# Kernel optimization log

Hardware: AMD Instinct MI355X
Metric: run time of the kernel (lower is better)

The kernel has to match this reference:

```python
import jax, jax.numpy as jnp
import numpy as np

T, B = 128, 256
E, H, C = 128, 1024, 10
VOCAB = 10


def setup_inputs() -> dict:
    key = jax.random.key(0)
    ks = jax.random.split(key, 12)
    x = jax.random.randint(ks[0], (T, B), 0, VOCAB)
    emb = jax.random.normal(ks[1], (VOCAB, E), dtype=jnp.float32)
    Wgx = jax.random.normal(ks[2], (E, H), dtype=jnp.float32) / np.sqrt(E)
    Wgh = jax.random.normal(ks[3], (H, H), dtype=jnp.float32) / np.sqrt(H)
    Wix = jax.random.normal(ks[4], (E, H), dtype=jnp.float32) / np.sqrt(E)
    Wih = jax.random.normal(ks[5], (H, H), dtype=jnp.float32) / np.sqrt(H)
    Wfx = jax.random.normal(ks[6], (E, H), dtype=jnp.float32) / np.sqrt(E)
    Wfh = jax.random.normal(ks[7], (H, H), dtype=jnp.float32) / np.sqrt(H)
    Wox = jax.random.normal(ks[8], (E, H), dtype=jnp.float32) / np.sqrt(E)
    Woh = jax.random.normal(ks[9], (H, H), dtype=jnp.float32) / np.sqrt(H)
    Wph = jax.random.normal(ks[10], (H, C), dtype=jnp.float32) / np.sqrt(H)
    bg = jnp.zeros((H,), jnp.float32)
    bi = jnp.zeros((H,), jnp.float32)
    bf = jnp.zeros((H,), jnp.float32)
    bo = jnp.zeros((H,), jnp.float32)
    bp = jnp.zeros((C,), jnp.float32)
    return dict(x=x, emb=emb, Wgx=Wgx, Wgh=Wgh, Wix=Wix, Wih=Wih, Wfx=Wfx,
                Wfh=Wfh, Wox=Wox, Woh=Woh, bg=bg, bi=bi, bf=bf, bo=bo,
                Wph=Wph, bp=bp)


def reference(x, emb, Wgx, Wgh, Wix, Wih, Wfx, Wfh, Wox, Woh,
              bg, bi, bf, bo, Wph, bp):
    Bsz = x.shape[1]
    Hn = Wgh.shape[0]
    # Fuse the 8 gate matmuls into 2 GEMMs per step (same math, concat order g,i,f,o)
    Wx = jnp.concatenate([Wgx, Wix, Wfx, Wox], axis=1)  # [E, 4H]
    Wh = jnp.concatenate([Wgh, Wih, Wfh, Woh], axis=1)  # [H, 4H]
    b = jnp.concatenate([bg, bi, bf, bo], axis=0)        # [4H]

    def step(carry, xt):
        state, hidden = carry
        e = emb[xt]                                      # [B, E]
        pre = e @ Wx + hidden @ Wh + b                   # [B, 4H]
        g = jnp.tanh(pre[:, :Hn])
        i = jax.nn.sigmoid(pre[:, Hn:2 * Hn])
        f = jax.nn.sigmoid(pre[:, 2 * Hn:3 * Hn])
        o = jax.nn.sigmoid(pre[:, 3 * Hn:])
        state = g * i + state * f
        hidden = jnp.tanh(state) * o
        return (state, hidden), None

    init = (jnp.zeros((Bsz, Hn), jnp.float32), jnp.zeros((Bsz, Hn), jnp.float32))
    (state, hidden), _ = jax.lax.scan(step, init, x)
    # Original detaches hidden/state before the output projection
    hidden = jax.lax.stop_gradient(hidden)
    return hidden @ Wph + bp                             # [B, C]
```

## Files before the change

kernel.cpp:

```cpp
#include <hip/hip_runtime.h>

typedef __bf16 bf16;
typedef __bf16 bf16x8 __attribute__((ext_vector_type(8)));
typedef float  f32x4  __attribute__((ext_vector_type(4)));
typedef int    i32x4  __attribute__((ext_vector_type(4)));

#define T_STEPS 128
#define BATCH   256
#define HD      1024
#define N4H     4096
#define EMB_D   128

#define MFMA_BF16(acc, Aop, Bop) \
    asm("v_mfma_f32_16x16x32_bf16 %0, %1, %2, %0" : "+v"(acc) : "a"(Aop), "v"(Bop))

__device__ __forceinline__ float fast_sigmoid(float x) {
    return 1.0f / (1.0f + __expf(-x));
}
__device__ __forceinline__ float fast_tanh(float x) {
    return 1.0f - 2.0f / (__expf(2.0f * x) + 1.0f);
}

__global__ void build_P(const float* __restrict__ emb,
                        const float* __restrict__ Wgx, const float* __restrict__ Wix,
                        const float* __restrict__ Wfx, const float* __restrict__ Wox,
                        const float* __restrict__ bg,  const float* __restrict__ bi,
                        const float* __restrict__ bfv, const float* __restrict__ bo,
                        float* __restrict__ P)
{
    int n = blockIdx.x * 256 + threadIdx.x;
    int v  = n >> 12;
    int nn = n & (N4H - 1);
    int hcol = nn >> 2, gate = nn & 3;
    const float* Wx = (gate == 0) ? Wgx : (gate == 1) ? Wix : (gate == 2) ? Wfx : Wox;
    const float* bb = (gate == 0) ? bg  : (gate == 1) ? bi  : (gate == 2) ? bfv : bo;
    float s = bb[hcol];
    for (int e = 0; e < EMB_D; ++e)
        s += emb[v * EMB_D + e] * Wx[e * HD + hcol];
    P[n] = s;
}

__global__ void build_W(const float* __restrict__ Wgh, const float* __restrict__ Wih,
                        const float* __restrict__ Wfh, const float* __restrict__ Woh,
                        bf16* __restrict__ WhpT)
{
    __shared__ float tile[64][65];
    int bid  = blockIdx.x;
    int gate = bid >> 8;
    int t2   = bid & 255;
    int kt = t2 >> 4, ht = t2 & 15;
    const float* W = (gate == 0) ? Wgh : (gate == 1) ? Wih : (gate == 2) ? Wfh : Woh;
    int tid = threadIdx.x;
    #pragma unroll
    for (int it = 0; it < 16; ++it) {
        int idx = it * 256 + tid;
        int kk = idx >> 6, hh = idx & 63;
        tile[kk][hh] = W[(size_t)(kt * 64 + kk) * HD + ht * 64 + hh];
    }
    __syncthreads();
    #pragma unroll
    for (int it = 0; it < 16; ++it) {
        int idx = it * 256 + tid;
        int hh = idx >> 6, kk = idx & 63;
        int n = (ht * 64 + hh) * 4 + gate;
        WhpT[(size_t)n * HD + kt * 64 + kk] = (bf16)tile[kk][hh];
    }
}

__global__ __launch_bounds__(512, 2)
void lstm_main(const int* __restrict__ x, const float* __restrict__ P,
               const bf16* __restrict__ WhpT, bf16* __restrict__ hbuf,
               int* __restrict__ ctl)
{
    __shared__ bf16  Blds[32][1024];
    __shared__ float red[8][64][9];
    __shared__ bf16  hst[32][34];
    __shared__ int   sj;

    const int tid  = threadIdx.x;
    const int lane = tid & 63;
    const int wid  = tid >> 6;
    const int w    = wid & 3;
    const int kh   = wid >> 2;
    const int frow = lane & 15;
    const int kgrp = lane >> 4;

    int xcc;
    asm("s_getreg_b32 %0, hwreg(HW_REG_XCC_ID)" : "=s"(xcc));
    const int g = xcc & 7;
    if (tid == 0)
        sj = __hip_atomic_fetch_add(ctl + 1024 + g * 16, 1,
                                    __ATOMIC_RELAXED, __HIP_MEMORY_SCOPE_AGENT) & 31;
    __syncthreads();
    const int j = sj;
    int* grpctr = ctl + g * 32;

    const int rowO = j * 128 + w * 32 + kh * 16 + frow;
    const int rowX = j * 128 + w * 32 + (1 - kh) * 16 + frow;
    const bf16* AbO = WhpT + (size_t)rowO * HD + kh * 512 + kgrp * 8;
    const bf16* AbX = WhpT + (size_t)rowX * HD + kh * 512 + kgrp * 8;
    i32x4 ArO[16], ArX[16];
    #pragma unroll
    for (int ks = 0; ks < 16; ++ks) {
        ArO[ks] = *(const i32x4*)(const void*)(AbO + ks * 32);
        ArX[ks] = *(const i32x4*)(const void*)(AbX + ks * 32);
    }
    #pragma unroll
    for (int ks = 0; ks < 16; ++ks)
        asm volatile("" : "+a"(ArO[ks]), "+a"(ArX[ks]));

    const int mr0 = g * 32 + frow;
    const int clc = w * 8 + kh * 4 + kgrp;
    const int pnb = j * 128 + clc * 4;
    const int xorf = frow & 7;
    char* BB = (char*)&Blds[0][0];
    float* rw = &red[0][0][0] + ((size_t)(wid ^ 4) * 64 + lane) * 9;
    const float* rr = &red[0][0][0] + ((size_t)wid * 64 + lane) * 9;
    const int* slot = grpctr + (lane & 31);

    float st0 = 0.f, st1 = 0.f;
    f32x4 accP0, accP1;
    {
        int xv0 = x[mr0], xv1 = x[mr0 + 16];
        accP0 = *(const f32x4*)(P + (size_t)xv0 * N4H + pnb);
        accP1 = *(const f32x4*)(P + (size_t)xv1 * N4H + pnb);
    }

    for (int t = 0; t < T_STEPS; ++t) {
        f32x4 accO0 = accP0, accO1 = accP1;
        f32x4 z = {0.f, 0.f, 0.f, 0.f};
        f32x4 accX0 = z, accX1 = z;

        if (t > 0) {
            if (wid == 0) {
                int cv; long guard = 0;
                do {
                    __builtin_amdgcn_s_sleep(1);
                    cv = __hip_atomic_load(slot, __ATOMIC_RELAXED,
                                           __HIP_MEMORY_SCOPE_AGENT);
                } while (!__all(cv >= t) && ++guard < (1L << 17));
            }
            __syncthreads();
            const char* src = (const char*)(hbuf + (size_t)(t & 1) * BATCH * HD
                                                 + (size_t)g * 32 * HD);
            f32x4 stg[8];
            #pragma unroll
            for (int i2 = 0; i2 < 8; ++i2)
                asm volatile("global_load_dwordx4 %0, %1, off sc0"
                             : "=v"(stg[i2]) : "v"(src + (i2 * 512 + tid) * 16));
            asm volatile("s_waitcnt vmcnt(0)" ::: "memory");
            #pragma unroll
            for (int i2 = 0; i2 < 8; ++i2) {
                int c = i2 * 512 + tid;
                int row = c >> 7, cg = c & 127;
                *(f32x4*)(BB + row * 2048 + ((cg ^ (row & 7)) << 4)) = stg[i2];
            }
            __syncthreads();
            #pragma unroll
            for (int ks = 0; ks < 16; ++ks) {
                int off = ((kh * 64 + ks * 4 + kgrp) ^ xorf) << 4;
                i32x4 b0 = *(const i32x4*)(BB + frow * 2048 + off);
                i32x4 b1 = *(const i32x4*)(BB + (frow + 16) * 2048 + off);
                MFMA_BF16(accO0, ArO[ks], b0);
                MFMA_BF16(accO1, ArO[ks], b1);
                MFMA_BF16(accX0, ArX[ks], b0);
                MFMA_BF16(accX1, ArX[ks], b1);
            }
        }

        rw[0] = accX0[0]; rw[1] = accX0[1]; rw[2] = accX0[2]; rw[3] = accX0[3];
        rw[4] = accX1[0]; rw[5] = accX1[1]; rw[6] = accX1[2]; rw[7] = accX1[3];
        __syncthreads();
        accO0[0] += rr[0]; accO0[1] += rr[1]; accO0[2] += rr[2]; accO0[3] += rr[3];
        accO1[0] += rr[4]; accO1[1] += rr[5]; accO1[2] += rr[6]; accO1[3] += rr[7];

        {
            float gg = fast_tanh(accO0[0]);
            float ii = fast_sigmoid(accO0[1]);
            float ff = fast_sigmoid(accO0[2]);
            float oo = fast_sigmoid(accO0[3]);
            float s = gg * ii + st0 * ff;
            st0 = s;
            hst[frow][clc] = (bf16)(fast_tanh(s) * oo);
        }
        {
            float gg = fast_tanh(accO1[0]);
            float ii = fast_sigmoid(accO1[1]);
            float ff = fast_sigmoid(accO1[2]);
            float oo = fast_sigmoid(accO1[3]);
            float s = gg * ii + st1 * ff;
            st1 = s;
            hst[frow + 16][clc] = (bf16)(fast_tanh(s) * oo);
        }

        if (t < T_STEPS - 1) {
            int xv0 = x[(t + 1) * BATCH + mr0], xv1 = x[(t + 1) * BATCH + mr0 + 16];
            accP0 = *(const f32x4*)(P + (size_t)xv0 * N4H + pnb);
            accP1 = *(const f32x4*)(P + (size_t)xv1 * N4H + pnb);
        }

        __syncthreads();
        {
            bf16* hout = hbuf + (size_t)((t + 1) & 1) * BATCH * HD;
            int r = tid >> 4, cp = (tid & 15) * 2;
            unsigned lo = (unsigned)__builtin_bit_cast(unsigned short, hst[r][cp]);
            unsigned hi = (unsigned)__builtin_bit_cast(unsigned short, hst[r][cp + 1]);
            unsigned pv = lo | (hi << 16);
            *(unsigned*)(hout + (size_t)(g * 32 + r) * HD + j * 32 + cp) = pv;
        }
        __syncthreads();
        if (tid == 0 && t < T_STEPS - 1)
            __hip_atomic_store(grpctr + j, t + 1,
                               __ATOMIC_RELAXED, __HIP_MEMORY_SCOPE_AGENT);
    }
}

__global__ void proj_out(const bf16* __restrict__ h, const float* __restrict__ Wph,
                         const float* __restrict__ bp, float* __restrict__ out)
{
    __shared__ float red[256][10];
    int b = blockIdx.x, tid = threadIdx.x;
    float acc[10];
    #pragma unroll
    for (int c = 0; c < 10; ++c) acc[c] = 0.f;
    for (int k = tid; k < HD; k += 256) {
        float hv = (float)h[(size_t)b * HD + k];
        #pragma unroll
        for (int c = 0; c < 10; ++c)
            acc[c] += hv * Wph[k * 10 + c];
    }
    #pragma unroll
    for (int c = 0; c < 10; ++c) red[tid][c] = acc[c];
    __syncthreads();
    for (int s = 128; s > 0; s >>= 1) {
        if (tid < s) {
            #pragma unroll
            for (int c = 0; c < 10; ++c) red[tid][c] += red[tid + s][c];
        }
        __syncthreads();
    }
    if (tid < 10) out[b * 10 + tid] = red[0][tid] + bp[tid];
}

extern "C" void kernel_launch(void* const* d_in, const int* in_sizes, int n_in,
                              void* d_out, int out_size, void* d_ws, size_t ws_size,
                              hipStream_t stream)
{
    const int*   x   = (const int*)  d_in[0];
    const float* emb = (const float*)d_in[1];
    const float* Wgx = (const float*)d_in[2];
    const float* Wgh = (const float*)d_in[3];
    const float* Wix = (const float*)d_in[4];
    const float* Wih = (const float*)d_in[5];
    const float* Wfx = (const float*)d_in[6];
    const float* Wfh = (const float*)d_in[7];
    const float* Wox = (const float*)d_in[8];
    const float* Woh = (const float*)d_in[9];
    const float* bg  = (const float*)d_in[10];
    const float* bi  = (const float*)d_in[11];
    const float* bfv = (const float*)d_in[12];
    const float* bo  = (const float*)d_in[13];
    const float* Wph = (const float*)d_in[14];
    const float* bp  = (const float*)d_in[15];

    char* ws = (char*)d_ws;
    bf16*  WhpT = (bf16*)ws;
    float* P    = (float*)(ws + 8388608);
    bf16*  hbuf = (bf16*)(ws + 8388608 + 163840);
    int*   ctl  = (int*)(ws + 8388608 + 163840 + 1048576);

    hipMemsetAsync(ctl, 0, 8192, stream);
    build_P<<<160, 256, 0, stream>>>(emb, Wgx, Wix, Wfx, Wox, bg, bi, bfv, bo, P);
    build_W<<<1024, 256, 0, stream>>>(Wgh, Wih, Wfh, Woh, WhpT);

    void* args[] = { (void*)&x, (void*)&P, (void*)&WhpT, (void*)&hbuf, (void*)&ctl };
    hipLaunchCooperativeKernel((void*)lstm_main, dim3(256), dim3(512), args, 0, stream);

    proj_out<<<256, 256, 0, stream>>>(hbuf, Wph, bp, (float*)d_out);
}
```

Baseline: 555.2 us.

## Split h staging by K-half and replace block barrier with per-half LDS flags

Each half of the workgroup (kh) now loads only the K-half of the hidden state that its own waves consume. Instead of a full __syncthreads after staging, the four waves in a half signal each other through per-wave LDS flags and spin on them. The s_sleep in the global poll loop is also removed to cut wake-up latency. The costs are busy-spinning waves competing for issue slots and reliance on LDS visibility ordering through volatile accesses and lgkmcnt waits.

```diff
diff --git a/kernel.cpp b/kernel.cpp
--- a/kernel.cpp
+++ b/kernel.cpp
@@ -75,6 +75,7 @@
     __shared__ bf16  Blds[32][1024];
     __shared__ float red[8][64][9];
     __shared__ bf16  hst[32][34];
+    __shared__ int   tflag[8];
     __shared__ int   sj;
 
     const int tid  = threadIdx.x;
@@ -84,6 +85,7 @@
     const int kh   = wid >> 2;
     const int frow = lane & 15;
     const int kgrp = lane >> 4;
+    const int ttid = tid & 255;
 
     int xcc;
     asm("s_getreg_b32 %0, hwreg(HW_REG_XCC_ID)" : "=s"(xcc));
@@ -91,6 +93,7 @@
     if (tid == 0)
         sj = __hip_atomic_fetch_add(ctl + 1024 + g * 16, 1,
                                     __ATOMIC_RELAXED, __HIP_MEMORY_SCOPE_AGENT) & 31;
+    if (tid < 8) tflag[tid] = 0;
     __syncthreads();
     const int j = sj;
     int* grpctr = ctl + g * 32;
@@ -135,7 +138,6 @@
             if (wid == 0) {
                 int cv; long guard = 0;
                 do {
-                    __builtin_amdgcn_s_sleep(1);
                     cv = __hip_atomic_load(slot, __ATOMIC_RELAXED,
                                            __HIP_MEMORY_SCOPE_AGENT);
                 } while (!__all(cv >= t) && ++guard < (1L << 17));
@@ -145,17 +147,32 @@
                                                  + (size_t)g * 32 * HD);
             f32x4 stg[8];
             #pragma unroll
-            for (int i2 = 0; i2 < 8; ++i2)
+            for (int it = 0; it < 8; ++it) {
+                int idx = it * 256 + ttid;
+                int row = idx >> 6, gg = idx & 63;
                 asm volatile("global_load_dwordx4 %0, %1, off sc0"
-                             : "=v"(stg[i2]) : "v"(src + (i2 * 512 + tid) * 16));
+                             : "=v"(stg[it])
+                             : "v"(src + row * 2048 + (kh * 64 + gg) * 16));
+            }
             asm volatile("s_waitcnt vmcnt(0)" ::: "memory");
             #pragma unroll
-            for (int i2 = 0; i2 < 8; ++i2) {
-                int c = i2 * 512 + tid;
-                int row = c >> 7, cg = c & 127;
-                *(f32x4*)(BB + row * 2048 + ((cg ^ (row & 7)) << 4)) = stg[i2];
-            }
-            __syncthreads();
+            for (int it = 0; it < 8; ++it) {
+                int idx = it * 256 + ttid;
+                int row = idx >> 6, gg = idx & 63;
+                int gl = kh * 64 + gg;
+                *(f32x4*)(BB + row * 2048 + ((gl ^ (row & 7)) << 4)) = stg[it];
+            }
+            asm volatile("s_waitcnt lgkmcnt(0)" ::: "memory");
+            if (lane == 0) ((volatile int*)tflag)[wid] = t;
+            {
+                volatile int* fb = (volatile int*)&tflag[kh * 4];
+                long guard = 0;
+                int f0, f1, f2, f3;
+                do {
+                    f0 = fb[0]; f1 = fb[1]; f2 = fb[2]; f3 = fb[3];
+                } while ((f0 < t || f1 < t || f2 < t || f3 < t)
+                         && ++guard < (1L << 17));
+            }
             #pragma unroll
             for (int ks = 0; ks < 16; ++ks) {
                 int off = ((kh * 64 + ks * 4 + kgrp) ^ xorf) << 4;
```

Result: no change. 558.9 us (+0.7%).

## Split batch into two ping-pong phases with per-phase counters and direct global B loads

Applied to the files above, without the earlier changes.

Each timestep is split into two half-batch phases (16 rows each), each with its own group counter array, so one half's recurrent exchange can overlap the other half's compute. The B operand is now loaded straight from global memory into registers with staged vmcnt waits interleaved with MFMAs, replacing the LDS staging buffer. The polling loop drops s_sleep, runs in all waves, and is skipped when a counter value prefetched during the previous phase already satisfies the condition. A 64KB dummy shared array is added, apparently to hold occupancy at one block per CU. The cost is twice as many barriers and flag publications per step, plus redundant global reads of h by every wave.

```diff
diff --git a/kernel.cpp b/kernel.cpp
--- a/kernel.cpp
+++ b/kernel.cpp
@@ -13,6 +13,13 @@
 
 #define MFMA_BF16(acc, Aop, Bop) \
     asm("v_mfma_f32_16x16x32_bf16 %0, %1, %2, %0" : "+v"(acc) : "a"(Aop), "v"(Bop))
+
+#define GA(i, OFF) asm volatile("global_load_dwordx4 %0, %1, off offset:" OFF " sc0" \
+                                : "=v"(bb[i]) : "v"(gsrc));
+#define CO(i, VM, AO, AX) \
+    asm volatile("s_waitcnt vmcnt(" VM ")" : "+v"(bb[i]) :: "memory"); \
+    MFMA_BF16(AO, ArO[i], bb[i]); \
+    MFMA_BF16(AX, ArX[i], bb[i]);
 
 __device__ __forceinline__ float fast_sigmoid(float x) {
     return 1.0f / (1.0f + __expf(-x));
@@ -72,10 +79,10 @@
                const bf16* __restrict__ WhpT, bf16* __restrict__ hbuf,
                int* __restrict__ ctl)
 {
-    __shared__ bf16  Blds[32][1024];
     __shared__ float red[8][64][9];
-    __shared__ bf16  hst[32][34];
+    __shared__ bf16  hst[16][34];
     __shared__ int   sj;
+    __shared__ char  pad[65536];
 
     const int tid  = threadIdx.x;
     const int lane = tid & 63;
@@ -84,6 +91,8 @@
     const int kh   = wid >> 2;
     const int frow = lane & 15;
     const int kgrp = lane >> 4;
+
+    if (blockDim.y == 2) pad[tid] = 1;
 
     int xcc;
     asm("s_getreg_b32 %0, hwreg(HW_REG_XCC_ID)" : "=s"(xcc));
@@ -93,7 +102,10 @@
                                     __ATOMIC_RELAXED, __HIP_MEMORY_SCOPE_AGENT) & 31;
     __syncthreads();
     const int j = sj;
-    int* grpctr = ctl + g * 32;
+    int* ctrA = ctl + (g * 2 + 0) * 32;
+    int* ctrB = ctl + (g * 2 + 1) * 32;
+    const int* slotA = ctrA + (lane & 31);
+    const int* slotB = ctrB + (lane & 31);
 
     const int rowO = j * 128 + w * 32 + kh * 16 + frow;
     const int rowX = j * 128 + w * 32 + (1 - kh) * 16 + frow;
@@ -109,109 +121,91 @@
     for (int ks = 0; ks < 16; ++ks)
         asm volatile("" : "+a"(ArO[ks]), "+a"(ArX[ks]));
 
-    const int mr0 = g * 32 + frow;
     const int clc = w * 8 + kh * 4 + kgrp;
     const int pnb = j * 128 + clc * 4;
-    const int xorf = frow & 7;
-    char* BB = (char*)&Blds[0][0];
+    const int mrA = g * 32 + frow;
+    const int mrB = g * 32 + 16 + frow;
     float* rw = &red[0][0][0] + ((size_t)(wid ^ 4) * 64 + lane) * 9;
     const float* rr = &red[0][0][0] + ((size_t)wid * 64 + lane) * 9;
-    const int* slot = grpctr + (lane & 31);
-
-    float st0 = 0.f, st1 = 0.f;
-    f32x4 accP0, accP1;
+
+    float stA = 0.f, stB = 0.f;
+    f32x4 accPA, accPB;
+    { int xv = x[mrA]; accPA = *(const f32x4*)(P + (size_t)xv * N4H + pnb); }
+    { int xv = x[mrB]; accPB = *(const f32x4*)(P + (size_t)xv * N4H + pnb); }
+    int cvPreA = 0, cvPreB = 0;
+
+    auto phase = [&](int t, int p, const int* slot, int* ctr, const int* slotOther,
+                     f32x4& accP, float& st, int mr, int& cvPreSelf, int& cvPreOther)
     {
-        int xv0 = x[mr0], xv1 = x[mr0 + 16];
-        accP0 = *(const f32x4*)(P + (size_t)xv0 * N4H + pnb);
-        accP1 = *(const f32x4*)(P + (size_t)xv1 * N4H + pnb);
-    }
-
-    for (int t = 0; t < T_STEPS; ++t) {
-        f32x4 accO0 = accP0, accO1 = accP1;
         f32x4 z = {0.f, 0.f, 0.f, 0.f};
-        f32x4 accX0 = z, accX1 = z;
+        f32x4 accOa = accP, accOb = z, accXa = z, accXb = z;
 
         if (t > 0) {
-            if (wid == 0) {
+            if (!__all(cvPreSelf >= t)) {
                 int cv; long guard = 0;
                 do {
-                    __builtin_amdgcn_s_sleep(1);
                     cv = __hip_atomic_load(slot, __ATOMIC_RELAXED,
                                            __HIP_MEMORY_SCOPE_AGENT);
                 } while (!__all(cv >= t) && ++guard < (1L << 17));
             }
-            __syncthreads();
-            const char* src = (const char*)(hbuf + (size_t)(t & 1) * BATCH * HD
-                                                 + (size_t)g * 32 * HD);
-            f32x4 stg[8];
-            #pragma unroll
-            for (int i2 = 0; i2 < 8; ++i2)
-                asm volatile("global_load_dwordx4 %0, %1, off sc0"
-                             : "=v"(stg[i2]) : "v"(src + (i2 * 512 + tid) * 16));
-            asm volatile("s_waitcnt vmcnt(0)" ::: "memory");
-            #pragma unroll
-            for (int i2 = 0; i2 < 8; ++i2) {
-                int c = i2 * 512 + tid;
-                int row = c >> 7, cg = c & 127;
-                *(f32x4*)(BB + row * 2048 + ((cg ^ (row & 7)) << 4)) = stg[i2];
-            }
-            __syncthreads();
-            #pragma unroll
-            for (int ks = 0; ks < 16; ++ks) {
-                int off = ((kh * 64 + ks * 4 + kgrp) ^ xorf) << 4;
-                i32x4 b0 = *(const i32x4*)(BB + frow * 2048 + off);
-                i32x4 b1 = *(const i32x4*)(BB + (frow + 16) * 2048 + off);
-                MFMA_BF16(accO0, ArO[ks], b0);
-                MFMA_BF16(accO1, ArO[ks], b1);
-                MFMA_BF16(accX0, ArX[ks], b0);
-                MFMA_BF16(accX1, ArX[ks], b1);
-            }
-        }
-
-        rw[0] = accX0[0]; rw[1] = accX0[1]; rw[2] = accX0[2]; rw[3] = accX0[3];
-        rw[4] = accX1[0]; rw[5] = accX1[1]; rw[6] = accX1[2]; rw[7] = accX1[3];
-        __syncthreads();
-        accO0[0] += rr[0]; accO0[1] += rr[1]; accO0[2] += rr[2]; accO0[3] += rr[3];
-        accO1[0] += rr[4]; accO1[1] += rr[5]; accO1[2] += rr[6]; accO1[3] += rr[7];
+            const bf16* gp = hbuf + (size_t)(t & 1) * BATCH * HD
+                                  + (size_t)mr * HD + kh * 512 + kgrp * 8;
+            const char* gsrc = (const char*)gp;
+            i32x4 bb[16];
+            GA(0,"0")   GA(1,"64")  GA(2,"128") GA(3,"192")
+            GA(4,"256") GA(5,"320") GA(6,"384") GA(7,"448")
+            CO(0,"7",accOa,accXa) CO(1,"6",accOb,accXb)
+            CO(2,"5",accOa,accXa) CO(3,"4",accOb,accXb)
+            GA(8,"512") GA(9,"576") GA(10,"640") GA(11,"704")
+            CO(4,"7",accOa,accXa) CO(5,"6",accOb,accXb)
+            CO(6,"5",accOa,accXa) CO(7,"4",accOb,accXb)
+            GA(12,"768") GA(13,"832") GA(14,"896") GA(15,"960")
+            CO(8,"7",accOa,accXa)  CO(9,"6",accOb,accXb)
+            CO(10,"5",accOa,accXa) CO(11,"4",accOb,accXb)
+            CO(12,"3",accOa,accXa) CO(13,"2",accOb,accXb)
+            CO(14,"1",accOa,accXa) CO(15,"0",accOb,accXb)
+        }
+        f32x4 accO = accOa + accOb;
+        f32x4 accX = accXa + accXb;
+
+        rw[0] = accX[0]; rw[1] = accX[1]; rw[2] = accX[2]; rw[3] = accX[3];
+        __syncthreads();
+        accO[0] += rr[0]; accO[1] += rr[1]; accO[2] += rr[2]; accO[3] += rr[3];
+
+        cvPreOther = __hip_atomic_load(slotOther, __ATOMIC_RELAXED,
+                                       __HIP_MEMORY_SCOPE_AGENT);
 
         {
-            float gg = fast_tanh(accO0[0]);
-            float ii = fast_sigmoid(accO0[1]);
-            float ff = fast_sigmoid(accO0[2]);
-            float oo = fast_sigmoid(accO0[3]);
-            float s = gg * ii + st0 * ff;
-            st0 = s;
+            float gg = fast_tanh(accO[0]);
+            float ii = fast_sigmoid(accO[1]);
+            float ff = fast_sigmoid(accO[2]);
+            float oo = fast_sigmoid(accO[3]);
+            float s = gg * ii + st * ff;
+            st = s;
             hst[frow][clc] = (bf16)(fast_tanh(s) * oo);
         }
-        {
-            float gg = fast_tanh(accO1[0]);
-            float ii = fast_sigmoid(accO1[1]);
-            float ff = fast_sigmoid(accO1[2]);
-            float oo = fast_sigmoid(accO1[3]);
-            float s = gg * ii + st1 * ff;
-            st1 = s;
-            hst[frow + 16][clc] = (bf16)(fast_tanh(s) * oo);
-        }
-
         if (t < T_STEPS - 1) {
-            int xv0 = x[(t + 1) * BATCH + mr0], xv1 = x[(t + 1) * BATCH + mr0 + 16];
-            accP0 = *(const f32x4*)(P + (size_t)xv0 * N4H + pnb);
-            accP1 = *(const f32x4*)(P + (size_t)xv1 * N4H + pnb);
-        }
-
-        __syncthreads();
-        {
+            int xv = x[(t + 1) * BATCH + mr];
+            accP = *(const f32x4*)(P + (size_t)xv * N4H + pnb);
+        }
+        __syncthreads();
+        if (tid < 256) {
             bf16* hout = hbuf + (size_t)((t + 1) & 1) * BATCH * HD;
             int r = tid >> 4, cp = (tid & 15) * 2;
             unsigned lo = (unsigned)__builtin_bit_cast(unsigned short, hst[r][cp]);
             unsigned hi = (unsigned)__builtin_bit_cast(unsigned short, hst[r][cp + 1]);
             unsigned pv = lo | (hi << 16);
-            *(unsigned*)(hout + (size_t)(g * 32 + r) * HD + j * 32 + cp) = pv;
+            *(unsigned*)(hout + (size_t)(g * 32 + p * 16 + r) * HD + j * 32 + cp) = pv;
         }
         __syncthreads();
         if (tid == 0 && t < T_STEPS - 1)
-            __hip_atomic_store(grpctr + j, t + 1,
+            __hip_atomic_store(ctr + j, t + 1,
                                __ATOMIC_RELAXED, __HIP_MEMORY_SCOPE_AGENT);
+    };
+
+    for (int t = 0; t < T_STEPS; ++t) {
+        phase(t, 0, slotA, ctrA, slotB, accPA, stA, mrA, cvPreA, cvPreB);
+        phase(t, 1, slotB, ctrB, slotA, accPB, stB, mrB, cvPreB, cvPreA);
     }
 }
 
```

After: 1.196 ms. 2.15x slower.
